# Kernel optimization log

Measured on AMD Instinct MI355X. Metric: run time of the kernel, lower is better.

The kernel has to match this reference:

```python
import jax, jax.numpy as jnp
import numpy as np

N_NODES = 50000


def _gat_layer(h, e_feat, Ww, Wb, aw, ab, src, dst):
    # h: [N,1,din], e_feat: [E,1,edim]
    hs = h[src]                                   # [E,1,din] gather src
    hd = h[dst]                                   # [E,1,din] gather dst
    # edge attention logit: relu(attn_fc(cat(src,dst)))
    e = jax.nn.relu(jnp.concatenate([hs, hd], axis=-1) @ aw.T + ab)  # [E,1,1]
    # segment softmax over incoming edges of each dst node
    emax = jax.ops.segment_max(e, dst, num_segments=N_NODES)          # [N,1,1]
    ex = jnp.exp(e - emax[dst])
    denom = jax.ops.segment_sum(ex, dst, num_segments=N_NODES)        # [N,1,1]
    alpha = ex / denom[dst]                                           # [E,1,1]
    # weighted scatter-sum of edge messages (m = edge features)
    z = jax.ops.segment_sum(alpha * e_feat, dst, num_segments=N_NODES)  # [N,1,edim]
    # node update: relu(W_apply(cat(h, z)))
    return jax.nn.relu(jnp.concatenate([h, z], axis=-1) @ Ww.T + Wb)    # [N,1,dout]


def setup_inputs() -> dict:
    key = jax.random.key(0)
    ks = jax.random.split(key, 12)
    N, E, D = N_NODES, 640000, 128
    s = 0.05  # weight scale for numerical sanity
    return {
        "nfeats": jax.random.normal(ks[0], (N, 1, D), jnp.float32),
        "efeats": jax.random.normal(ks[1], (E, 1, D), jnp.float32),
        "W_apply_w0": jax.random.normal(ks[2], (D, 2 * D), jnp.float32) * s,
        "W_apply_b0": jax.random.normal(ks[3], (D,), jnp.float32) * s,
        "attn_w0": jax.random.normal(ks[4], (1, 2 * D), jnp.float32) * s,
        "attn_b0": jax.random.normal(ks[5], (1,), jnp.float32) * s,
        "W_apply_w1": jax.random.normal(ks[6], (D, 2 * D), jnp.float32) * s,
        "W_apply_b1": jax.random.normal(ks[7], (D,), jnp.float32) * s,
        "attn_w1": jax.random.normal(ks[8], (1, 2 * D), jnp.float32) * s,
        "attn_b1": jax.random.normal(ks[9], (1,), jnp.float32) * s,
        "src": jax.random.randint(ks[10], (E,), 0, N, jnp.int32),
        "dst": jax.random.randint(ks[11], (E,), 0, N, jnp.int32),
    }


def reference(nfeats, efeats, W_apply_w0, W_apply_b0, attn_w0, attn_b0,
              W_apply_w1, W_apply_b1, attn_w1, attn_b1, src, dst):
    h = _gat_layer(nfeats, efeats, W_apply_w0, W_apply_b0, attn_w0, attn_b0, src, dst)
    # dropout is identity in eval mode
    h = _gat_layer(h, efeats, W_apply_w1, W_apply_b1, attn_w1, attn_b1, src, dst)
    return h.sum(axis=1)  # [N, dout]
```

## Files before the change

kernel.cpp:

```cpp
#include <hip/hip_runtime.h>


__global__ void hist_k(const int* __restrict__ dst, int* __restrict__ counts, int E){
  int e = blockIdx.x*blockDim.x + threadIdx.x;
  if(e<E) atomicAdd(&counts[dst[e]], 1);
}

__global__ __launch_bounds__(1024) void scan1_k(const int* __restrict__ counts, int* __restrict__ excl,
                                                int* __restrict__ partials, int N){
  __shared__ int tmp[1024];
  int tid = threadIdx.x;
  int i = blockIdx.x*1024 + tid;
  int v = (i<N)? counts[i] : 0;
  tmp[tid] = v;
  __syncthreads();
  for(int off=1; off<1024; off<<=1){
    int t = (tid>=off)? tmp[tid-off] : 0;
    __syncthreads();
    tmp[tid] += t;
    __syncthreads();
  }
  if(i<N) excl[i] = tmp[tid] - v;
  if(tid==1023) partials[blockIdx.x] = tmp[tid];
}

__global__ void scan2_k(int* __restrict__ partials, int NB){
  __shared__ int tmp[64];
  int tid = threadIdx.x;
  int v = (tid<NB)? partials[tid] : 0;
  tmp[tid] = v;
  __syncthreads();
  for(int off=1; off<64; off<<=1){
    int t = (tid>=off)? tmp[tid-off] : 0;
    __syncthreads();
    tmp[tid] += t;
    __syncthreads();
  }
  if(tid<NB) partials[tid] = tmp[tid] - v;
}

__global__ __launch_bounds__(1024) void scan3_k(int* __restrict__ row_ptr, const int* __restrict__ partials,
                                                int* __restrict__ cursors, int N, int E){
  int i = blockIdx.x*1024 + threadIdx.x;
  if(i<N){
    int r = row_ptr[i] + partials[blockIdx.x];
    row_ptr[i] = r;
    cursors[i] = r;
  }
  if(i==0) row_ptr[N] = E;
}

__global__ void scatter_k(const int* __restrict__ src, const int* __restrict__ dst, int* __restrict__ cursors,
                          int* __restrict__ eperm, int* __restrict__ esrc, int E){
  int e = blockIdx.x*blockDim.x + threadIdx.x;
  if(e<E){
    int d = dst[e];
    int p = atomicAdd(&cursors[d], 1);
    eperm[p] = e;
    esrc[p] = src[e];
  }
}


__global__ void attn_k(const float* __restrict__ h, const float* __restrict__ aw, const float* __restrict__ ab,
                       float* __restrict__ a_src, float* __restrict__ a_dst, int N){
  int gid = blockIdx.x*blockDim.x + threadIdx.x;
  int n = gid >> 6, lane = gid & 63;
  if(n >= N) return;
  float2 hv = ((const float2*)(h + (size_t)n*128))[lane];
  float2 wa = ((const float2*)aw)[lane];
  float2 wb = ((const float2*)(aw+128))[lane];
  float s = hv.x*wa.x + hv.y*wa.y;
  float t = hv.x*wb.x + hv.y*wb.y;
  #pragma unroll
  for(int off=32; off>0; off>>=1){
    s += __shfl_xor(s, off, 64);
    t += __shfl_xor(t, off, 64);
  }
  if(lane==0){ a_src[n] = s; a_dst[n] = t + ab[0]; }
}

__global__ __launch_bounds__(256) void agg_k(const float* __restrict__ efeats,
    const float* __restrict__ a_src, const float* __restrict__ a_dst,
    const int* __restrict__ row_ptr, const int* __restrict__ eperm, const int* __restrict__ esrc,
    float* __restrict__ z, int N){
  int gid = blockIdx.x*blockDim.x + threadIdx.x;
  int n = gid >> 6, lane = gid & 63;
  if(n >= N) return;
  int beg = row_ptr[n], end = row_ptr[n+1];
  int deg = end - beg;
  float2 acc; acc.x = 0.f; acc.y = 0.f;
  if(deg <= 0){ ((float2*)z)[(size_t)n*64 + lane] = acc; return; }
  float adn = a_dst[n];

  int i = beg + lane;
  bool valid = i < end;
  int perm_reg = valid ? eperm[i] : 0;
  float e_reg = valid ? fmaxf(a_src[esrc[i]] + adn, 0.f) : -1e30f;

  float m = e_reg;
  #pragma unroll
  for(int off=32; off>0; off>>=1) m = fmaxf(m, __shfl_xor(m, off, 64));
  for(int c = beg + 64; c < end; c += 64){
    int ii = c + lane;
    float ev = (ii < end) ? fmaxf(a_src[esrc[ii]] + adn, 0.f) : -1e30f;
    #pragma unroll
    for(int off=32; off>0; off>>=1) ev = fmaxf(ev, __shfl_xor(ev, off, 64));
    m = fmaxf(m, ev);
  }

  float ex_reg = valid ? __expf(e_reg - m) : 0.f;
  float s = ex_reg;
  #pragma unroll
  for(int off=32; off>0; off>>=1) s += __shfl_xor(s, off, 64);
  for(int c = beg + 64; c < end; c += 64){
    int ii = c + lane;
    float ev = (ii < end) ? __expf(fmaxf(a_src[esrc[ii]] + adn, 0.f) - m) : 0.f;
    #pragma unroll
    for(int off=32; off>0; off>>=1) ev += __shfl_xor(ev, off, 64);
    s += ev;
  }
  float inv = 1.f / s;

  const float2* ef2 = (const float2*)efeats;
  int cnt = min(deg, 64);
  int j = 0;
  for(; j + 4 <= cnt; j += 4){
    float p0 = __shfl(ex_reg, j+0, 64); int r0 = __shfl(perm_reg, j+0, 64);
    float p1 = __shfl(ex_reg, j+1, 64); int r1 = __shfl(perm_reg, j+1, 64);
    float p2 = __shfl(ex_reg, j+2, 64); int r2 = __shfl(perm_reg, j+2, 64);
    float p3 = __shfl(ex_reg, j+3, 64); int r3 = __shfl(perm_reg, j+3, 64);
    float2 f0 = ef2[(size_t)r0*64 + lane];
    float2 f1 = ef2[(size_t)r1*64 + lane];
    float2 f2 = ef2[(size_t)r2*64 + lane];
    float2 f3 = ef2[(size_t)r3*64 + lane];
    acc.x += p0*f0.x; acc.y += p0*f0.y;
    acc.x += p1*f1.x; acc.y += p1*f1.y;
    acc.x += p2*f2.x; acc.y += p2*f2.y;
    acc.x += p3*f3.x; acc.y += p3*f3.y;
  }
  for(; j < cnt; j++){
    float p = __shfl(ex_reg, j, 64); int r = __shfl(perm_reg, j, 64);
    float2 f = ef2[(size_t)r*64 + lane];
    acc.x += p*f.x; acc.y += p*f.y;
  }
  for(int c = beg + 64; c < end; c += 64){
    int ii = c + lane;
    bool v2 = ii < end;
    int pr = v2 ? eperm[ii] : 0;
    float er = v2 ? __expf(fmaxf(a_src[esrc[ii]] + adn, 0.f) - m) : 0.f;
    int cc = min(end - c, 64);
    for(int jj = 0; jj < cc; jj++){
      float p = __shfl(er, jj, 64); int r = __shfl(pr, jj, 64);
      float2 f = ef2[(size_t)r*64 + lane];
      acc.x += p*f.x; acc.y += p*f.y;
    }
  }

  acc.x *= inv; acc.y *= inv;
  ((float2*)z)[(size_t)n*64 + lane] = acc;
}

__global__ __launch_bounds__(256) void update_k(const float* __restrict__ h, const float* __restrict__ z,
                                                const float* __restrict__ W, const float* __restrict__ bias,
                                                float* __restrict__ out, int N){
  __shared__ float xs[64][36];
  __shared__ float ws[32][132];
  int tid = threadIdx.x;
  int tx = tid & 15;
  int ty = tid >> 4;
  int n0 = blockIdx.x * 64;
  float acc[4][8];
  #pragma unroll
  for(int i=0;i<4;i++)
    #pragma unroll
    for(int j=0;j<8;j++) acc[i][j] = 0.f;

  int lr = tid >> 2;
  int lk = (tid & 3) * 8;
  int wo = tid >> 1;
  int wk = (tid & 1) * 16;

  for(int kb=0; kb<256; kb+=32){
    {
      int node = n0 + lr;
      float4 v0 = make_float4(0.f,0.f,0.f,0.f), v1 = v0;
      if(node < N){
        int kg = kb + lk;
        const float* sp = (kg < 128) ? (h + (size_t)node*128 + kg)
                                     : (z + (size_t)node*128 + (kg-128));
        v0 = ((const float4*)sp)[0];
        v1 = ((const float4*)sp)[1];
      }
      *(float4*)&xs[lr][lk]   = v0;
      *(float4*)&xs[lr][lk+4] = v1;
    }
    {
      const float* wp = W + (size_t)wo*256 + kb + wk;
      float4 a0 = ((const float4*)wp)[0];
      float4 a1 = ((const float4*)wp)[1];
      float4 a2 = ((const float4*)wp)[2];
      float4 a3 = ((const float4*)wp)[3];
      float vals[16] = {a0.x,a0.y,a0.z,a0.w, a1.x,a1.y,a1.z,a1.w,
                        a2.x,a2.y,a2.z,a2.w, a3.x,a3.y,a3.z,a3.w};
      #pragma unroll
      for(int j=0;j<16;j++) ws[wk+j][wo] = vals[j];
    }
    __syncthreads();
    #pragma unroll 8
    for(int k=0;k<32;k++){
      float xv[4];
      #pragma unroll
      for(int i=0;i<4;i++) xv[i] = xs[ty*4+i][k];
      float4 w0 = *(const float4*)&ws[k][tx*8];
      float4 w1 = *(const float4*)&ws[k][tx*8+4];
      float wv[8] = {w0.x,w0.y,w0.z,w0.w, w1.x,w1.y,w1.z,w1.w};
      #pragma unroll
      for(int i=0;i<4;i++)
        #pragma unroll
        for(int j=0;j<8;j++)
          acc[i][j] += xv[i]*wv[j];
    }
    __syncthreads();
  }

  const float4* b4 = (const float4*)bias;
  float4 bb0 = b4[tx*2], bb1 = b4[tx*2+1];
  #pragma unroll
  for(int i=0;i<4;i++){
    int n = n0 + ty*4 + i;
    if(n >= N) continue;
    float4 r0, r1;
    r0.x = fmaxf(acc[i][0]+bb0.x, 0.f);
    r0.y = fmaxf(acc[i][1]+bb0.y, 0.f);
    r0.z = fmaxf(acc[i][2]+bb0.z, 0.f);
    r0.w = fmaxf(acc[i][3]+bb0.w, 0.f);
    r1.x = fmaxf(acc[i][4]+bb1.x, 0.f);
    r1.y = fmaxf(acc[i][5]+bb1.y, 0.f);
    r1.z = fmaxf(acc[i][6]+bb1.z, 0.f);
    r1.w = fmaxf(acc[i][7]+bb1.w, 0.f);
    float4* op = (float4*)(out + (size_t)n*128 + tx*8);
    op[0] = r0; op[1] = r1;
  }
}


extern "C" void kernel_launch(void* const* d_in, const int* in_sizes, int n_in,
                              void* d_out, int out_size, void* d_ws, size_t ws_size,
                              hipStream_t stream){
  const float* nfeats = (const float*)d_in[0];
  const float* efeats = (const float*)d_in[1];
  const float* Ww0 = (const float*)d_in[2];
  const float* Wb0 = (const float*)d_in[3];
  const float* aw0 = (const float*)d_in[4];
  const float* ab0 = (const float*)d_in[5];
  const float* Ww1 = (const float*)d_in[6];
  const float* Wb1 = (const float*)d_in[7];
  const float* aw1 = (const float*)d_in[8];
  const float* ab1 = (const float*)d_in[9];
  const int* src = (const int*)d_in[10];
  const int* dst = (const int*)d_in[11];
  int E = in_sizes[10];
  int N = in_sizes[0] / 128;

  char* base = (char*)d_ws;
  size_t off = 0;
  auto take = [&](size_t bytes) -> char* {
    char* p = base + off;
    off = (off + bytes + 255) & ~(size_t)255;
    return p;
  };
  int*   counts  = (int*)take((size_t)N*4);
  int*   row_ptr = (int*)take((size_t)(N+1)*4);
  int*   cursors = (int*)take((size_t)N*4);
  int*   partials= (int*)take(256);
  int*   eperm   = (int*)take((size_t)E*4);
  int*   esrc    = (int*)take((size_t)E*4);
  float* a_src   = (float*)take((size_t)N*4);
  float* a_dst   = (float*)take((size_t)N*4);
  float* zbuf    = (float*)take((size_t)N*128*4);
  float* h1      = (float*)take((size_t)N*128*4);

  int NB = (N + 1023)/1024;

  hipMemsetAsync(counts, 0, (size_t)N*4, stream);
  hist_k<<<(E+255)/256, 256, 0, stream>>>(dst, counts, E);
  scan1_k<<<NB, 1024, 0, stream>>>(counts, row_ptr, partials, N);
  scan2_k<<<1, 64, 0, stream>>>(partials, NB);
  scan3_k<<<NB, 1024, 0, stream>>>(row_ptr, partials, cursors, N, E);
  scatter_k<<<(E+255)/256, 256, 0, stream>>>(src, dst, cursors, eperm, esrc, E);

  int agrid = (N + 3)/4;
  attn_k<<<agrid, 256, 0, stream>>>(nfeats, aw0, ab0, a_src, a_dst, N);
  agg_k<<<agrid, 256, 0, stream>>>(efeats, a_src, a_dst, row_ptr, eperm, esrc, zbuf, N);
  update_k<<<(N+63)/64, 256, 0, stream>>>(nfeats, zbuf, Ww0, Wb0, h1, N);
  attn_k<<<agrid, 256, 0, stream>>>(h1, aw1, ab1, a_src, a_dst, N);
  agg_k<<<agrid, 256, 0, stream>>>(efeats, a_src, a_dst, row_ptr, eperm, esrc, zbuf, N);
  update_k<<<(N+63)/64, 256, 0, stream>>>(h1, zbuf, Ww1, Wb1, (float*)d_out, N);
}
```

Before: 754.8 us.

## Pack edge indices, widen aggregation to float4 halves, retile update GEMM with prefetch

Edge permutation and source indices are packed into one int2 array so each edge needs a single load. The aggregation kernel now splits each wavefront into two 32-lane halves that process alternate edges with float4 loads and combine them with a cross-half shuffle. The update GEMM is retiled to 128 nodes per block with 8x8 register tiles, a pre-transposed weight matrix, and register prefetch of the next k-slice to overlap global loads with compute. The cost is extra register pressure in the GEMM and two small transpose kernels per call.

```diff
diff --git a/kernel.cpp b/kernel.cpp
--- a/kernel.cpp
+++ b/kernel.cpp
@@ -51,14 +51,19 @@
 }
 
 __global__ void scatter_k(const int* __restrict__ src, const int* __restrict__ dst, int* __restrict__ cursors,
-                          int* __restrict__ eperm, int* __restrict__ esrc, int E){
+                          int2* __restrict__ edat, int E){
   int e = blockIdx.x*blockDim.x + threadIdx.x;
   if(e<E){
     int d = dst[e];
     int p = atomicAdd(&cursors[d], 1);
-    eperm[p] = e;
-    esrc[p] = src[e];
-  }
+    edat[p] = make_int2(e, src[e]);
+  }
+}
+
+__global__ void wt_k(const float* __restrict__ W, float* __restrict__ Wt){
+  int idx = blockIdx.x*256 + threadIdx.x;
+  int k = idx >> 7, o = idx & 127;
+  Wt[idx] = W[o*256 + k];
 }
 
 
@@ -82,28 +87,32 @@
 
 __global__ __launch_bounds__(256) void agg_k(const float* __restrict__ efeats,
     const float* __restrict__ a_src, const float* __restrict__ a_dst,
-    const int* __restrict__ row_ptr, const int* __restrict__ eperm, const int* __restrict__ esrc,
+    const int* __restrict__ row_ptr, const int2* __restrict__ edat,
     float* __restrict__ z, int N){
   int gid = blockIdx.x*blockDim.x + threadIdx.x;
   int n = gid >> 6, lane = gid & 63;
   if(n >= N) return;
+  int half = lane >> 5, l32 = lane & 31;
   int beg = row_ptr[n], end = row_ptr[n+1];
   int deg = end - beg;
-  float2 acc; acc.x = 0.f; acc.y = 0.f;
-  if(deg <= 0){ ((float2*)z)[(size_t)n*64 + lane] = acc; return; }
+  if(deg <= 0){
+    if(half==0) ((float4*)z)[(size_t)n*32 + l32] = make_float4(0.f,0.f,0.f,0.f);
+    return;
+  }
   float adn = a_dst[n];
 
   int i = beg + lane;
   bool valid = i < end;
-  int perm_reg = valid ? eperm[i] : 0;
-  float e_reg = valid ? fmaxf(a_src[esrc[i]] + adn, 0.f) : -1e30f;
+  int2 es = valid ? edat[i] : make_int2(0,0);
+  int perm_reg = es.x;
+  float e_reg = valid ? fmaxf(a_src[es.y] + adn, 0.f) : -1e30f;
 
   float m = e_reg;
   #pragma unroll
   for(int off=32; off>0; off>>=1) m = fmaxf(m, __shfl_xor(m, off, 64));
   for(int c = beg + 64; c < end; c += 64){
     int ii = c + lane;
-    float ev = (ii < end) ? fmaxf(a_src[esrc[ii]] + adn, 0.f) : -1e30f;
+    float ev = (ii < end) ? fmaxf(a_src[edat[ii].y] + adn, 0.f) : -1e30f;
     #pragma unroll
     for(int off=32; off>0; off>>=1) ev = fmaxf(ev, __shfl_xor(ev, off, 64));
     m = fmaxf(m, ev);
@@ -115,120 +124,156 @@
   for(int off=32; off>0; off>>=1) s += __shfl_xor(s, off, 64);
   for(int c = beg + 64; c < end; c += 64){
     int ii = c + lane;
-    float ev = (ii < end) ? __expf(fmaxf(a_src[esrc[ii]] + adn, 0.f) - m) : 0.f;
+    float ev = (ii < end) ? __expf(fmaxf(a_src[edat[ii].y] + adn, 0.f) - m) : 0.f;
     #pragma unroll
     for(int off=32; off>0; off>>=1) ev += __shfl_xor(ev, off, 64);
     s += ev;
   }
   float inv = 1.f / s;
 
-  const float2* ef2 = (const float2*)efeats;
+  const float4* ef4 = (const float4*)efeats;
+  float4 acc = make_float4(0.f,0.f,0.f,0.f);
   int cnt = min(deg, 64);
   int j = 0;
-  for(; j + 4 <= cnt; j += 4){
-    float p0 = __shfl(ex_reg, j+0, 64); int r0 = __shfl(perm_reg, j+0, 64);
-    float p1 = __shfl(ex_reg, j+1, 64); int r1 = __shfl(perm_reg, j+1, 64);
-    float p2 = __shfl(ex_reg, j+2, 64); int r2 = __shfl(perm_reg, j+2, 64);
-    float p3 = __shfl(ex_reg, j+3, 64); int r3 = __shfl(perm_reg, j+3, 64);
-    float2 f0 = ef2[(size_t)r0*64 + lane];
-    float2 f1 = ef2[(size_t)r1*64 + lane];
-    float2 f2 = ef2[(size_t)r2*64 + lane];
-    float2 f3 = ef2[(size_t)r3*64 + lane];
-    acc.x += p0*f0.x; acc.y += p0*f0.y;
-    acc.x += p1*f1.x; acc.y += p1*f1.y;
-    acc.x += p2*f2.x; acc.y += p2*f2.y;
-    acc.x += p3*f3.x; acc.y += p3*f3.y;
-  }
-  for(; j < cnt; j++){
+  for(; j + 8 <= cnt; j += 8){
+    float p0 = __shfl(ex_reg, j+half,   64); int r0 = __shfl(perm_reg, j+half,   64);
+    float p1 = __shfl(ex_reg, j+2+half, 64); int r1 = __shfl(perm_reg, j+2+half, 64);
+    float p2 = __shfl(ex_reg, j+4+half, 64); int r2 = __shfl(perm_reg, j+4+half, 64);
+    float p3 = __shfl(ex_reg, j+6+half, 64); int r3 = __shfl(perm_reg, j+6+half, 64);
+    float4 f0 = ef4[(size_t)r0*32 + l32];
+    float4 f1 = ef4[(size_t)r1*32 + l32];
+    float4 f2 = ef4[(size_t)r2*32 + l32];
+    float4 f3 = ef4[(size_t)r3*32 + l32];
+    acc.x += p0*f0.x; acc.y += p0*f0.y; acc.z += p0*f0.z; acc.w += p0*f0.w;
+    acc.x += p1*f1.x; acc.y += p1*f1.y; acc.z += p1*f1.z; acc.w += p1*f1.w;
+    acc.x += p2*f2.x; acc.y += p2*f2.y; acc.z += p2*f2.z; acc.w += p2*f2.w;
+    acc.x += p3*f3.x; acc.y += p3*f3.y; acc.z += p3*f3.z; acc.w += p3*f3.w;
+  }
+  for(; j + 2 <= cnt; j += 2){
+    float p = __shfl(ex_reg, j+half, 64); int r = __shfl(perm_reg, j+half, 64);
+    float4 f = ef4[(size_t)r*32 + l32];
+    acc.x += p*f.x; acc.y += p*f.y; acc.z += p*f.z; acc.w += p*f.w;
+  }
+  if(j < cnt){
     float p = __shfl(ex_reg, j, 64); int r = __shfl(perm_reg, j, 64);
-    float2 f = ef2[(size_t)r*64 + lane];
-    acc.x += p*f.x; acc.y += p*f.y;
+    if(half==0){
+      float4 f = ef4[(size_t)r*32 + l32];
+      acc.x += p*f.x; acc.y += p*f.y; acc.z += p*f.z; acc.w += p*f.w;
+    }
   }
   for(int c = beg + 64; c < end; c += 64){
     int ii = c + lane;
     bool v2 = ii < end;
-    int pr = v2 ? eperm[ii] : 0;
-    float er = v2 ? __expf(fmaxf(a_src[esrc[ii]] + adn, 0.f) - m) : 0.f;
+    int2 es2 = v2 ? edat[ii] : make_int2(0,0);
+    int pr = es2.x;
+    float er = v2 ? __expf(fmaxf(a_src[es2.y] + adn, 0.f) - m) : 0.f;
     int cc = min(end - c, 64);
-    for(int jj = 0; jj < cc; jj++){
+    int jj = 0;
+    for(; jj + 2 <= cc; jj += 2){
+      float p = __shfl(er, jj+half, 64); int r = __shfl(pr, jj+half, 64);
+      float4 f = ef4[(size_t)r*32 + l32];
+      acc.x += p*f.x; acc.y += p*f.y; acc.z += p*f.z; acc.w += p*f.w;
+    }
+    if(jj < cc){
       float p = __shfl(er, jj, 64); int r = __shfl(pr, jj, 64);
-      float2 f = ef2[(size_t)r*64 + lane];
-      acc.x += p*f.x; acc.y += p*f.y;
-    }
-  }
-
-  acc.x *= inv; acc.y *= inv;
-  ((float2*)z)[(size_t)n*64 + lane] = acc;
+      if(half==0){
+        float4 f = ef4[(size_t)r*32 + l32];
+        acc.x += p*f.x; acc.y += p*f.y; acc.z += p*f.z; acc.w += p*f.w;
+      }
+    }
+  }
+
+  acc.x += __shfl_xor(acc.x, 32, 64);
+  acc.y += __shfl_xor(acc.y, 32, 64);
+  acc.z += __shfl_xor(acc.z, 32, 64);
+  acc.w += __shfl_xor(acc.w, 32, 64);
+  if(half==0){
+    acc.x *= inv; acc.y *= inv; acc.z *= inv; acc.w *= inv;
+    ((float4*)z)[(size_t)n*32 + l32] = acc;
+  }
 }
 
 __global__ __launch_bounds__(256) void update_k(const float* __restrict__ h, const float* __restrict__ z,
-                                                const float* __restrict__ W, const float* __restrict__ bias,
+                                                const float* __restrict__ Wt, const float* __restrict__ bias,
                                                 float* __restrict__ out, int N){
-  __shared__ float xs[64][36];
+  __shared__ float xsT[32][132];
   __shared__ float ws[32][132];
   int tid = threadIdx.x;
   int tx = tid & 15;
   int ty = tid >> 4;
-  int n0 = blockIdx.x * 64;
-  float acc[4][8];
-  #pragma unroll
-  for(int i=0;i<4;i++)
-    #pragma unroll
-    for(int j=0;j<8;j++) acc[i][j] = 0.f;
-
-  int lr = tid >> 2;
-  int lk = (tid & 3) * 8;
-  int wo = tid >> 1;
-  int wk = (tid & 1) * 16;
+  int n0 = blockIdx.x * 128;
+
+  int sn  = tid >> 1;
+  int skc = (tid & 1) * 16;
+  int wkk = tid >> 3;
+  int woc = (tid & 7) * 4;
+
+  float4 xv4[4], wv4[4];
+  {
+    int node = n0 + sn;
+    bool v = node < N;
+    const float* sp = h + (size_t)node*128 + skc;
+    #pragma unroll
+    for(int jj=0;jj<4;jj++) xv4[jj] = v ? ((const float4*)sp)[jj] : make_float4(0.f,0.f,0.f,0.f);
+    const float* wp = Wt + (size_t)wkk*128 + woc;
+    #pragma unroll
+    for(int jj=0;jj<4;jj++) wv4[jj] = *(const float4*)(wp + jj*32);
+  }
+
+  float acc[8][8];
+  #pragma unroll
+  for(int i=0;i<8;i++)
+    #pragma unroll
+    for(int j2=0;j2<8;j2++) acc[i][j2] = 0.f;
 
   for(int kb=0; kb<256; kb+=32){
-    {
-      int node = n0 + lr;
-      float4 v0 = make_float4(0.f,0.f,0.f,0.f), v1 = v0;
-      if(node < N){
-        int kg = kb + lk;
-        const float* sp = (kg < 128) ? (h + (size_t)node*128 + kg)
-                                     : (z + (size_t)node*128 + (kg-128));
-        v0 = ((const float4*)sp)[0];
-        v1 = ((const float4*)sp)[1];
-      }
-      *(float4*)&xs[lr][lk]   = v0;
-      *(float4*)&xs[lr][lk+4] = v1;
-    }
-    {
-      const float* wp = W + (size_t)wo*256 + kb + wk;
-      float4 a0 = ((const float4*)wp)[0];
-      float4 a1 = ((const float4*)wp)[1];
-      float4 a2 = ((const float4*)wp)[2];
-      float4 a3 = ((const float4*)wp)[3];
-      float vals[16] = {a0.x,a0.y,a0.z,a0.w, a1.x,a1.y,a1.z,a1.w,
-                        a2.x,a2.y,a2.z,a2.w, a3.x,a3.y,a3.z,a3.w};
+    #pragma unroll
+    for(int jj=0;jj<4;jj++){
+      int kq = skc + jj*4;
+      xsT[kq+0][sn] = xv4[jj].x;
+      xsT[kq+1][sn] = xv4[jj].y;
+      xsT[kq+2][sn] = xv4[jj].z;
+      xsT[kq+3][sn] = xv4[jj].w;
+      *(float4*)&ws[wkk][woc + jj*32] = wv4[jj];
+    }
+    __syncthreads();
+
+    if(kb + 32 < 256){
+      int kb2 = kb + 32;
+      int node = n0 + sn;
+      bool v = node < N;
+      const float* sp = (kb2 < 128) ? h + (size_t)node*128 + kb2 + skc
+                                    : z + (size_t)node*128 + (kb2-128) + skc;
       #pragma unroll
-      for(int j=0;j<16;j++) ws[wk+j][wo] = vals[j];
-    }
-    __syncthreads();
+      for(int jj=0;jj<4;jj++) xv4[jj] = v ? ((const float4*)sp)[jj] : make_float4(0.f,0.f,0.f,0.f);
+      const float* wp = Wt + (size_t)(kb2 + wkk)*128 + woc;
+      #pragma unroll
+      for(int jj=0;jj<4;jj++) wv4[jj] = *(const float4*)(wp + jj*32);
+    }
+
     #pragma unroll 8
     for(int k=0;k<32;k++){
-      float xv[4];
-      #pragma unroll
-      for(int i=0;i<4;i++) xv[i] = xs[ty*4+i][k];
-      float4 w0 = *(const float4*)&ws[k][tx*8];
-      float4 w1 = *(const float4*)&ws[k][tx*8+4];
+      float4 x0 = *(const float4*)&xsT[k][ty*4];
+      float4 x1 = *(const float4*)&xsT[k][64 + ty*4];
+      float4 w0 = *(const float4*)&ws[k][tx*4];
+      float4 w1 = *(const float4*)&ws[k][64 + tx*4];
+      float xv[8] = {x0.x,x0.y,x0.z,x0.w, x1.x,x1.y,x1.z,x1.w};
       float wv[8] = {w0.x,w0.y,w0.z,w0.w, w1.x,w1.y,w1.z,w1.w};
       #pragma unroll
-      for(int i=0;i<4;i++)
+      for(int i=0;i<8;i++)
         #pragma unroll
-        for(int j=0;j<8;j++)
-          acc[i][j] += xv[i]*wv[j];
+        for(int j2=0;j2<8;j2++)
+          acc[i][j2] += xv[i]*wv[j2];
     }
     __syncthreads();
   }
 
   const float4* b4 = (const float4*)bias;
-  float4 bb0 = b4[tx*2], bb1 = b4[tx*2+1];
-  #pragma unroll
-  for(int i=0;i<4;i++){
-    int n = n0 + ty*4 + i;
+  float4 bb0 = b4[tx];
+  float4 bb1 = b4[16 + tx];
+  #pragma unroll
+  for(int i=0;i<8;i++){
+    int n = n0 + ((i<4) ? (ty*4 + i) : (64 + ty*4 + (i-4)));
     if(n >= N) continue;
     float4 r0, r1;
     r0.x = fmaxf(acc[i][0]+bb0.x, 0.f);
@@ -239,8 +284,8 @@
     r1.y = fmaxf(acc[i][5]+bb1.y, 0.f);
     r1.z = fmaxf(acc[i][6]+bb1.z, 0.f);
     r1.w = fmaxf(acc[i][7]+bb1.w, 0.f);
-    float4* op = (float4*)(out + (size_t)n*128 + tx*8);
-    op[0] = r0; op[1] = r1;
+    *(float4*)(out + (size_t)n*128 + tx*4)      = r0;
+    *(float4*)(out + (size_t)n*128 + 64 + tx*4) = r1;
   }
 }
 
@@ -274,27 +319,31 @@
   int*   row_ptr = (int*)take((size_t)(N+1)*4);
   int*   cursors = (int*)take((size_t)N*4);
   int*   partials= (int*)take(256);
-  int*   eperm   = (int*)take((size_t)E*4);
-  int*   esrc    = (int*)take((size_t)E*4);
+  int2*  edat    = (int2*)take((size_t)E*8);
   float* a_src   = (float*)take((size_t)N*4);
   float* a_dst   = (float*)take((size_t)N*4);
   float* zbuf    = (float*)take((size_t)N*128*4);
   float* h1      = (float*)take((size_t)N*128*4);
+  float* Wt0     = (float*)take((size_t)256*128*4);
+  float* Wt1     = (float*)take((size_t)256*128*4);
 
   int NB = (N + 1023)/1024;
 
   hipMemsetAsync(counts, 0, (size_t)N*4, stream);
+  wt_k<<<128, 256, 0, stream>>>(Ww0, Wt0);
+  wt_k<<<128, 256, 0, stream>>>(Ww1, Wt1);
   hist_k<<<(E+255)/256, 256, 0, stream>>>(dst, counts, E);
   scan1_k<<<NB, 1024, 0, stream>>>(counts, row_ptr, partials, N);
   scan2_k<<<1, 64, 0, stream>>>(partials, NB);
   scan3_k<<<NB, 1024, 0, stream>>>(row_ptr, partials, cursors, N, E);
-  scatter_k<<<(E+255)/256, 256, 0, stream>>>(src, dst, cursors, eperm, esrc, E);
+  scatter_k<<<(E+255)/256, 256, 0, stream>>>(src, dst, cursors, edat, E);
 
   int agrid = (N + 3)/4;
+  int ugrid = (N + 127)/128;
   attn_k<<<agrid, 256, 0, stream>>>(nfeats, aw0, ab0, a_src, a_dst, N);
-  agg_k<<<agrid, 256, 0, stream>>>(efeats, a_src, a_dst, row_ptr, eperm, esrc, zbuf, N);
-  update_k<<<(N+63)/64, 256, 0, stream>>>(nfeats, zbuf, Ww0, Wb0, h1, N);
+  agg_k<<<agrid, 256, 0, stream>>>(efeats, a_src, a_dst, row_ptr, edat, zbuf, N);
+  update_k<<<ugrid, 256, 0, stream>>>(nfeats, zbuf, Wt0, Wb0, h1, N);
   attn_k<<<agrid, 256, 0, stream>>>(h1, aw1, ab1, a_src, a_dst, N);
-  agg_k<<<agrid, 256, 0, stream>>>(efeats, a_src, a_dst, row_ptr, eperm, esrc, zbuf, N);
-  update_k<<<(N+63)/64, 256, 0, stream>>>(h1, zbuf, Ww1, Wb1, (float*)d_out, N);
-}
+  agg_k<<<agrid, 256, 0, stream>>>(efeats, a_src, a_dst, row_ptr, edat, zbuf, N);
+  update_k<<<ugrid, 256, 0, stream>>>(h1, zbuf, Wt1, Wb1, (float*)d_out, N);
+}
```

After: 773.8 us. 1.03x slower.
